# Optimization experiments

Measured on AMD Instinct MI355X. Metric: run time of the kernel, lower is better.

## Reference

```python
import jax, jax.numpy as jnp
import numpy as np

B, N, IN_DIM, OUT_DIM, H = 8, 1024, 512, 512, 8
SUP = OUT_DIM // H  # support_dim per head = 64


def setup_inputs() -> dict:
    key = jax.random.key(0)
    ks = jax.random.split(key, 6)
    # 0/1 dense adjacency with self-loops so no row is fully masked
    A = jax.random.randint(ks[0], (B, N, N), 0, 2).astype(jnp.float32)
    A = jnp.maximum(A, jnp.eye(N, dtype=jnp.float32)[None])
    X = jax.random.normal(ks[1], (B, N, IN_DIM), dtype=jnp.float32)
    # parameters, uniform(-1/sqrt(fan_last), 1/sqrt(fan_last)) as in reset_parameters
    sw = 1.0 / np.sqrt(SUP)
    W = jax.random.uniform(ks[2], (H, IN_DIM, SUP), minval=-sw, maxval=sw, dtype=jnp.float32)
    w1 = jax.random.uniform(ks[3], (H, SUP), minval=-sw, maxval=sw, dtype=jnp.float32)
    w2 = jax.random.uniform(ks[4], (H, SUP), minval=-sw, maxval=sw, dtype=jnp.float32)
    b = jax.random.uniform(ks[5], (2, H), minval=-1.0, maxval=1.0, dtype=jnp.float32)
    b1, b2 = b[0], b[1]
    return {"A": A, "X": X, "W": W, "w1": w1, "b1": b1, "w2": w2, "b2": b2}


def reference(A, X, W, w1, b1, w2, b2):
    # per-head projection: [B,H,N,SUP]
    inputs = jnp.einsum('bni,hio->bhno', X, W)
    # additive attention logits: self_fc [B,H,N,1] + neigh_fc [B,H,1,N]
    self_fc = jnp.einsum('bhno,ho->bhn', inputs, w1) + b1[None, :, None]
    neigh_fc = jnp.einsum('bhno,ho->bhn', inputs, w2) + b2[None, :, None]
    logits = jax.nn.leaky_relu(self_fc[..., :, None] + neigh_fc[..., None, :], 0.01)
    mask = -1e9 * (1.0 - A)  # [B,N,N]
    alphas = jax.nn.softmax(logits + mask[:, None], axis=-1)  # [B,H,N,N]
    out = jnp.einsum('bhnm,bhmo->bhno', alphas, inputs)
    out = jax.nn.relu(out)  # default activation = torch.relu
    # concat heads on last dim (head i contiguous), matching torch.cat
    return out.transpose(0, 2, 1, 3).reshape(B, N, H * SUP)
```

## Files before the change

### kernel.cpp

```cpp
#include <hip/hip_runtime.h>
#include <hip/hip_fp16.h>

#define BB 8
#define NN 1024
#define IN_DIM 512
#define HH 8
#define SUP 64
#define HS (HH * SUP)

#define XS_STRIDE 40
#define VT2 1032

typedef _Float16 half8 __attribute__((ext_vector_type(8)));
typedef _Float16 half2v __attribute__((ext_vector_type(2)));
typedef float floatx4 __attribute__((ext_vector_type(4)));

__global__ __launch_bounds__(256) void kW(const float* __restrict__ W,
                                          _Float16* __restrict__ Wt) {
    __shared__ float tile[64][65];
    const int it = blockIdx.x & 7;
    const int h  = blockIdx.x >> 3;
    const int t  = threadIdx.x;
    {
        const int i  = t >> 2;
        const int o0 = (t & 3) * 16;
        const float* src = W + ((size_t)h * IN_DIM + it * 64 + i) * SUP + o0;
#pragma unroll
        for (int j = 0; j < 4; j++) {
            float4 v = ((const float4*)src)[j];
            tile[i][o0 + j * 4 + 0] = v.x;
            tile[i][o0 + j * 4 + 1] = v.y;
            tile[i][o0 + j * 4 + 2] = v.z;
            tile[i][o0 + j * 4 + 3] = v.w;
        }
    }
    __syncthreads();
    {
        const int o  = t >> 2;
        const int i0 = (t & 3) * 16;
        _Float16 buf[16];
#pragma unroll
        for (int j = 0; j < 16; j++) buf[j] = (_Float16)tile[i0 + j][o];
        _Float16* dst = Wt + ((size_t)h * SUP + o) * IN_DIM + it * 64 + i0;
        *(half8*)dst       = *(half8*)buf;
        *(half8*)(dst + 8) = *(half8*)(buf + 8);
    }
}

__global__ __launch_bounds__(256) void k1_proj(const float* __restrict__ X,
                                               const _Float16* __restrict__ Wt,
                                               const float* __restrict__ A,
                                               unsigned char* __restrict__ Am,
                                               const float* __restrict__ w1,
                                               const float* __restrict__ b1,
                                               const float* __restrict__ w2,
                                               const float* __restrict__ b2,
                                               _Float16* __restrict__ Pt,
                                               float* __restrict__ s_g,
                                               float* __restrict__ t_g,
                                               float* __restrict__ tmax16) {
    __shared__ __align__(16) _Float16 xs[2][64 * XS_STRIDE];
    __shared__ __align__(16) _Float16 wsh[2][128 * XS_STRIDE];
    __shared__ __align__(16) _Float16 po[128 * 72];
    __shared__ float tred[2][64];

    const int bid  = blockIdx.x;
    const int t    = threadIdx.x;
    const int wave = t >> 6;
    const int lane = t & 63;

    if (bid >= 512) {
        const int idx = bid - 512;
#pragma unroll
        for (int i = 0; i < 8; i++) {
            const int row = idx * 32 + wave * 8 + i;
            const float* arow = A + (size_t)row * NN;
            unsigned long long keep = 0;
#pragma unroll
            for (int g = 0; g < 16; g++) {
                float a = arow[g * 64 + lane];
                unsigned long long bal = __ballot(a > 0.5f);
                if (lane == g) keep = bal;
            }
            if (lane < 16)
                *(unsigned long long*)(Am + (size_t)row * 128 + lane * 8) = keep;
        }
        return;
    }

    const int b    = bid & 7;
    const int j    = bid >> 3;
    const int h0   = (j & 3) * 2;
    const int bh0  = b * 8 + h0;
    const int n0   = (j >> 2) * 64;
    const int quad = lane >> 4;
    const int l15  = lane & 15;
    const int row  = t >> 2;
    const int koff = (t & 3) * 8;
    const int wrow  = t >> 1;
    const int wkoff = (t & 1) * 16;

    floatx4 acc[8];
#pragma unroll
    for (int i = 0; i < 8; i++) acc[i] = {0.f, 0.f, 0.f, 0.f};

    float w1v[8], w2v[8];
#pragma unroll
    for (int ct = 0; ct < 8; ct++) {
        w1v[ct] = w1[h0 * 64 + ct * 16 + l15];
        w2v[ct] = w2[h0 * 64 + ct * 16 + l15];
    }
    const float b1h0 = b1[h0], b1h1 = b1[h0 + 1];
    const float b2h0 = b2[h0], b2h1 = b2[h0 + 1];

    const float*    xbase = X + ((size_t)b * NN + n0 + row) * IN_DIM + koff;
    const _Float16* wbase = Wt + ((size_t)(h0 * SUP) + wrow) * IN_DIM + wkoff;

    float4 xa = ((const float4*)xbase)[0];
    float4 xb = ((const float4*)xbase)[1];
    half8  wv0 = ((const half8*)wbase)[0];
    half8  wv1 = *(const half8*)(wbase + 8);

    for (int it = 0; it < 16; it++) {
        const int cur = it & 1;
        {
            _Float16 xh[8] = {(_Float16)xa.x, (_Float16)xa.y, (_Float16)xa.z, (_Float16)xa.w,
                              (_Float16)xb.x, (_Float16)xb.y, (_Float16)xb.z, (_Float16)xb.w};
            *(half8*)&xs[cur][row * XS_STRIDE + koff] = *(half8*)xh;
            *(half8*)&wsh[cur][wrow * XS_STRIDE + wkoff]     = wv0;
            *(half8*)&wsh[cur][wrow * XS_STRIDE + wkoff + 8] = wv1;
        }
        __syncthreads();
        if (it < 15) {
            const float* src = xbase + (it + 1) * 32;
            xa = ((const float4*)src)[0];
            xb = ((const float4*)src)[1];
            wv0 = *(const half8*)(wbase + (it + 1) * 32);
            wv1 = *(const half8*)(wbase + (it + 1) * 32 + 8);
        }
        half8 af = *(const half8*)&xs[cur][(wave * 16 + l15) * XS_STRIDE + quad * 8];
#pragma unroll
        for (int ct = 0; ct < 8; ct++) {
            half8 bf = *(const half8*)&wsh[cur][(ct * 16 + l15) * XS_STRIDE + quad * 8];
            acc[ct] = __builtin_amdgcn_mfma_f32_16x16x32_f16(af, bf, acc[ct], 0, 0, 0);
        }
    }
    __syncthreads();

#pragma unroll
    for (int ct = 0; ct < 8; ct++) {
#pragma unroll
        for (int r = 0; r < 4; r++) {
            int o = ct * 16 + l15;
            int n = wave * 16 + quad * 4 + r;
            po[o * 72 + n] = (_Float16)acc[ct][r];
        }
    }
#pragma unroll
    for (int r = 0; r < 4; r++) {
        float sp0 = 0.f, tp0 = 0.f, sp1 = 0.f, tp1 = 0.f;
#pragma unroll
        for (int ct = 0; ct < 4; ct++) {
            sp0 += acc[ct][r] * w1v[ct];
            tp0 += acc[ct][r] * w2v[ct];
            sp1 += acc[ct + 4][r] * w1v[ct + 4];
            tp1 += acc[ct + 4][r] * w2v[ct + 4];
        }
#pragma unroll
        for (int off = 1; off < 16; off <<= 1) {
            sp0 += __shfl_xor(sp0, off);
            tp0 += __shfl_xor(tp0, off);
            sp1 += __shfl_xor(sp1, off);
            tp1 += __shfl_xor(tp1, off);
        }
        if (l15 == 0) {
            const int n = wave * 16 + quad * 4 + r;
            s_g[(size_t)bh0 * NN + n0 + n] = sp0 + b1h0;
            float tv0 = tp0 + b2h0;
            t_g[(size_t)bh0 * NN + n0 + n] = tv0;
            tred[0][n] = tv0;
            s_g[(size_t)(bh0 + 1) * NN + n0 + n] = sp1 + b1h1;
            float tv1 = tp1 + b2h1;
            t_g[(size_t)(bh0 + 1) * NN + n0 + n] = tv1;
            tred[1][n] = tv1;
        }
    }
    __syncthreads();
    {
        const int orow = t >> 1;
        const int nof  = (t & 1) * 32;
        _Float16* dst = Pt + ((size_t)(bh0 * SUP + orow)) * NN + n0 + nof;
        const _Float16* src = &po[orow * 72 + nof];
        *(half8*)dst        = *(const half8*)src;
        *(half8*)(dst + 8)  = *(const half8*)(src + 8);
        *(half8*)(dst + 16) = *(const half8*)(src + 16);
        *(half8*)(dst + 24) = *(const half8*)(src + 24);
    }
    if (t == 0) {
        float m0 = -1e30f, m1 = -1e30f;
#pragma unroll
        for (int i = 0; i < 64; i++) {
            m0 = fmaxf(m0, tred[0][i]);
            m1 = fmaxf(m1, tred[1][i]);
        }
        tmax16[bh0 * 16 + (n0 >> 6)] = m0;
        tmax16[(bh0 + 1) * 16 + (n0 >> 6)] = m1;
    }
}

__global__ __launch_bounds__(1024) void k2_attn(const unsigned char* __restrict__ Am,
                                                const _Float16* __restrict__ Pt,
                                                const float* __restrict__ s_g,
                                                const float* __restrict__ t_g,
                                                const float* __restrict__ tmax16,
                                                float* __restrict__ out) {
    __shared__ __align__(16) _Float16 vts[64 * VT2];
    __shared__ __align__(16) unsigned t2l[NN / 2];
    __shared__ __align__(16) uint4 lutm[256];

    const int bid  = blockIdx.x;
    const int b    = bid & 7;
    const int rest = bid >> 3;
    const int h    = rest & 7;
    const int bh   = b * 8 + h;
    const int n0   = (rest >> 3) * 256;
    const int t    = threadIdx.x;
    const int wave = t >> 6;
    const int lane = t & 63;
    const int quad = lane >> 4;
    const int l15  = lane & 15;

    {
        const int tt   = t & 511;
        const int half = t >> 9;
        const int row4 = tt >> 3;
        const int seg  = tt & 7;
        const _Float16* src = Pt + ((size_t)bh * SUP + row4) * NN + half * 512 + seg * 16;
        _Float16*       dst = &vts[row4 * VT2 + half * 512 + seg * 16];
        half8 r0[4], r1[4];
#pragma unroll
        for (int m = 0; m < 4; m++) {
            r0[m] = ((const half8*)(src + m * 128))[0];
            r1[m] = ((const half8*)(src + m * 128))[1];
        }
#pragma unroll
        for (int m = 0; m < 4; m++) {
            ((half8*)(dst + m * 128))[0] = r0[m];
            ((half8*)(dst + m * 128))[1] = r1[m];
        }
    }
    if (t < 512) {
        float2 tv2 = ((const float2*)(t_g + (size_t)bh * NN))[t];
        half2v tp = {(_Float16)tv2.x, (_Float16)tv2.y};
        t2l[t] = *(unsigned*)&tp;
    }
    if (t < 256) {
        unsigned e = (unsigned)t;
        uint4 v;
        v.x = ((e & 1u)   ? 0xFFFFu : 0u) | ((e & 2u)   ? 0xFFFF0000u : 0u);
        v.y = ((e & 4u)   ? 0xFFFFu : 0u) | ((e & 8u)   ? 0xFFFF0000u : 0u);
        v.z = ((e & 16u)  ? 0xFFFFu : 0u) | ((e & 32u)  ? 0xFFFF0000u : 0u);
        v.w = ((e & 64u)  ? 0xFFFFu : 0u) | ((e & 128u) ? 0xFFFF0000u : 0u);
        lutm[t] = v;
    }

    float tmax = -1e30f;
#pragma unroll
    for (int i = 0; i < 16; i++) tmax = fmaxf(tmax, tmax16[bh * 16 + i]);

    const int myrow = wave * 16 + l15;
    const float sv = s_g[(size_t)bh * NN + n0 + myrow];
    const float xc = sv + tmax;
    const float cv = fmaxf(xc, 0.01f * xc);
    const float l2e = 1.44269504f;
    const _Float16 sc1h = (_Float16)((sv - cv) * l2e);
    const _Float16 sc2h = (_Float16)(-0.99f * cv * l2e);
    const half2v sc1 = {sc1h, sc1h};
    const half2v sc2 = {sc2h, sc2h};
    const half2v vl2e = {(_Float16)l2e, (_Float16)l2e};
    const half2v v001 = {(_Float16)0.01f, (_Float16)0.01f};
    const half2v ones2 = {(_Float16)1.0f, (_Float16)1.0f};

    floatx4 acc[4];
#pragma unroll
    for (int i = 0; i < 4; i++) acc[i] = {0.f, 0.f, 0.f, 0.f};
    float zp = 0.f;

    const uint4* mrow = (const uint4*)(Am + ((size_t)b * NN + n0 + myrow) * 128);
    uint4 mcur = mrow[0];

    __syncthreads();

    for (int mt = 0; mt < 8; mt++) {
        uint4 mnext;
        if (mt < 7) mnext = mrow[mt + 1];
        const unsigned mw[4] = {mcur.x, mcur.y, mcur.z, mcur.w};
#pragma unroll
        for (int kk = 0; kk < 4; kk++) {
            const unsigned mbyte = (mw[kk] >> (quad * 8)) & 0xffu;
            uint4 mx = lutm[mbyte];
            const unsigned mxw[4] = {mx.x, mx.y, mx.z, mx.w};
            uint4 tw = *(const uint4*)&t2l[mt * 64 + kk * 16 + quad * 4];
            union { uint4 u; half2v h[4]; } tt; tt.u = tw;
            union { half2v h[4]; half8 h8; } wbu;
#pragma unroll
            for (int p = 0; p < 4; p++) {
                half2v y = tt.h[p] * vl2e + sc1;
                half2v w = y * v001 + sc2;
                half2v z = __builtin_elementwise_max(y, w);
                __half2 zz = *(__half2*)&z;
                __half2 ee = h2exp2(zz);
                unsigned eb = (*(unsigned*)&ee) & mxw[p];
                half2v e2 = *(half2v*)&eb;
#if __has_builtin(__builtin_amdgcn_fdot2)
                zp = __builtin_amdgcn_fdot2(e2, ones2, zp, false);
#else
                zp += (float)e2.x + (float)e2.y;
#endif
                wbu.h[p] = e2;
            }
            half8 af = wbu.h8;
#pragma unroll
            for (int ct = 0; ct < 4; ct++) {
                half8 bf = *(const half8*)&vts[(ct * 16 + l15) * VT2 + mt * 128 + kk * 32 + quad * 8];
                acc[ct] = __builtin_amdgcn_mfma_f32_16x16x32_f16(af, bf, acc[ct], 0, 0, 0);
            }
        }
        if (mt < 7) mcur = mnext;
    }

    zp += __shfl_xor(zp, 16);
    zp += __shfl_xor(zp, 32);
    const float rzown = 1.0f / zp;

#pragma unroll
    for (int r = 0; r < 4; r++) {
        const int rr = wave * 16 + quad * 4 + r;
        const float rz = __shfl(rzown, quad * 20 + r);
#pragma unroll
        for (int ct = 0; ct < 4; ct++) {
            float v = acc[ct][r] * rz;
            v = v > 0.f ? v : 0.f;
            out[((size_t)b * NN + n0 + rr) * HS + h * SUP + ct * 16 + l15] = v;
        }
    }
}

extern "C" void kernel_launch(void* const* d_in, const int* in_sizes, int n_in,
                              void* d_out, int out_size, void* d_ws, size_t ws_size,
                              hipStream_t stream) {
    const float* A  = (const float*)d_in[0];
    const float* X  = (const float*)d_in[1];
    const float* W  = (const float*)d_in[2];
    const float* w1 = (const float*)d_in[3];
    const float* b1 = (const float*)d_in[4];
    const float* w2 = (const float*)d_in[5];
    const float* b2 = (const float*)d_in[6];
    float* out = (float*)d_out;

    char* ws = (char*)d_ws;
    _Float16*      Wt     = (_Float16*)(ws);
    _Float16*      Pt     = (_Float16*)(ws + 524288);
    float*         s_g    = (float*)(ws + 8912896);
    float*         t_g    = (float*)(ws + 9175040);
    float*         tmax16 = (float*)(ws + 9437184);
    unsigned char* Am     = (unsigned char*)(ws + 9441280);

    hipLaunchKernelGGL(kW, dim3(64), dim3(256), 0, stream, W, Wt);
    hipLaunchKernelGGL(k1_proj, dim3(768), dim3(256), 0, stream,
                       X, Wt, A, Am, w1, b1, w2, b2, Pt, s_g, t_g, tmax16);
    hipLaunchKernelGGL(k2_attn, dim3(256), dim3(1024), 0, stream,
                       Am, Pt, s_g, t_g, tmax16, out);
}
```

Before: 130.5 us.

## Shrink projection LDS via aliasing, unroll K-loop by two, compute masks arithmetically

In the projection kernel, the double-buffered X/W staging and the output tile now share one aliased LDS array, and the kernel gets a min-blocks-per-CU launch bound of 4 to raise occupancy. The K loop is manually unrolled into two buffers with two prefetch register sets in flight. In the attention kernel, the 256-entry LDS mask lookup table is replaced by shift-based sign extension that builds each half2 mask word in registers. This removes an LDS gather per step and the table setup, at the cost of a few extra ALU ops. The larger prefetch register set could raise pressure under the tighter launch bound.

```diff
diff --git a/kernel.cpp b/kernel.cpp
--- a/kernel.cpp
+++ b/kernel.cpp
@@ -47,22 +47,25 @@
     }
 }
 
-__global__ __launch_bounds__(256) void k1_proj(const float* __restrict__ X,
-                                               const _Float16* __restrict__ Wt,
-                                               const float* __restrict__ A,
-                                               unsigned char* __restrict__ Am,
-                                               const float* __restrict__ w1,
-                                               const float* __restrict__ b1,
-                                               const float* __restrict__ w2,
-                                               const float* __restrict__ b2,
-                                               _Float16* __restrict__ Pt,
-                                               float* __restrict__ s_g,
-                                               float* __restrict__ t_g,
-                                               float* __restrict__ tmax16) {
-    __shared__ __align__(16) _Float16 xs[2][64 * XS_STRIDE];
-    __shared__ __align__(16) _Float16 wsh[2][128 * XS_STRIDE];
-    __shared__ __align__(16) _Float16 po[128 * 72];
+__global__ __launch_bounds__(256, 4) void k1_proj(const float* __restrict__ X,
+                                                  const _Float16* __restrict__ Wt,
+                                                  const float* __restrict__ A,
+                                                  unsigned char* __restrict__ Am,
+                                                  const float* __restrict__ w1,
+                                                  const float* __restrict__ b1,
+                                                  const float* __restrict__ w2,
+                                                  const float* __restrict__ b2,
+                                                  _Float16* __restrict__ Pt,
+                                                  float* __restrict__ s_g,
+                                                  float* __restrict__ t_g,
+                                                  float* __restrict__ tmax16) {
+    __shared__ __align__(16) _Float16 sm[15360];
     __shared__ float tred[2][64];
+    _Float16* const xs0 = sm;
+    _Float16* const xs1 = sm + 2560;
+    _Float16* const ws0 = sm + 5120;
+    _Float16* const ws1 = sm + 10240;
+    _Float16* const po  = sm;
 
     const int bid  = blockIdx.x;
     const int t    = threadIdx.x;
@@ -116,33 +119,64 @@
     const float*    xbase = X + ((size_t)b * NN + n0 + row) * IN_DIM + koff;
     const _Float16* wbase = Wt + ((size_t)(h0 * SUP) + wrow) * IN_DIM + wkoff;
 
-    float4 xa = ((const float4*)xbase)[0];
-    float4 xb = ((const float4*)xbase)[1];
-    half8  wv0 = ((const half8*)wbase)[0];
-    half8  wv1 = *(const half8*)(wbase + 8);
-
-    for (int it = 0; it < 16; it++) {
-        const int cur = it & 1;
+    float4 xaA = ((const float4*)xbase)[0];
+    float4 xbA = ((const float4*)xbase)[1];
+    half8  wv0A = *(const half8*)(wbase);
+    half8  wv1A = *(const half8*)(wbase + 8);
+    float4 xaB = ((const float4*)(xbase + 32))[0];
+    float4 xbB = ((const float4*)(xbase + 32))[1];
+    half8  wv0B = *(const half8*)(wbase + 32);
+    half8  wv1B = *(const half8*)(wbase + 40);
+
+    const int afoff = (wave * 16 + l15) * XS_STRIDE + quad * 8;
+
+#pragma unroll 1
+    for (int jj = 0; jj < 8; jj++) {
         {
-            _Float16 xh[8] = {(_Float16)xa.x, (_Float16)xa.y, (_Float16)xa.z, (_Float16)xa.w,
-                              (_Float16)xb.x, (_Float16)xb.y, (_Float16)xb.z, (_Float16)xb.w};
-            *(half8*)&xs[cur][row * XS_STRIDE + koff] = *(half8*)xh;
-            *(half8*)&wsh[cur][wrow * XS_STRIDE + wkoff]     = wv0;
-            *(half8*)&wsh[cur][wrow * XS_STRIDE + wkoff + 8] = wv1;
+            _Float16 xh[8] = {(_Float16)xaA.x, (_Float16)xaA.y, (_Float16)xaA.z, (_Float16)xaA.w,
+                              (_Float16)xbA.x, (_Float16)xbA.y, (_Float16)xbA.z, (_Float16)xbA.w};
+            *(half8*)&xs0[row * XS_STRIDE + koff] = *(half8*)xh;
+            *(half8*)&ws0[wrow * XS_STRIDE + wkoff]     = wv0A;
+            *(half8*)&ws0[wrow * XS_STRIDE + wkoff + 8] = wv1A;
         }
         __syncthreads();
-        if (it < 15) {
-            const float* src = xbase + (it + 1) * 32;
-            xa = ((const float4*)src)[0];
-            xb = ((const float4*)src)[1];
-            wv0 = *(const half8*)(wbase + (it + 1) * 32);
-            wv1 = *(const half8*)(wbase + (it + 1) * 32 + 8);
-        }
-        half8 af = *(const half8*)&xs[cur][(wave * 16 + l15) * XS_STRIDE + quad * 8];
-#pragma unroll
-        for (int ct = 0; ct < 8; ct++) {
-            half8 bf = *(const half8*)&wsh[cur][(ct * 16 + l15) * XS_STRIDE + quad * 8];
-            acc[ct] = __builtin_amdgcn_mfma_f32_16x16x32_f16(af, bf, acc[ct], 0, 0, 0);
+        if (jj < 7) {
+            const float* src = xbase + (2 * jj + 2) * 32;
+            xaA = ((const float4*)src)[0];
+            xbA = ((const float4*)src)[1];
+            wv0A = *(const half8*)(wbase + (2 * jj + 2) * 32);
+            wv1A = *(const half8*)(wbase + (2 * jj + 2) * 32 + 8);
+        }
+        {
+            half8 af = *(const half8*)&xs0[afoff];
+#pragma unroll
+            for (int ct = 0; ct < 8; ct++) {
+                half8 bf = *(const half8*)&ws0[(ct * 16 + l15) * XS_STRIDE + quad * 8];
+                acc[ct] = __builtin_amdgcn_mfma_f32_16x16x32_f16(af, bf, acc[ct], 0, 0, 0);
+            }
+        }
+        {
+            _Float16 xh[8] = {(_Float16)xaB.x, (_Float16)xaB.y, (_Float16)xaB.z, (_Float16)xaB.w,
+                              (_Float16)xbB.x, (_Float16)xbB.y, (_Float16)xbB.z, (_Float16)xbB.w};
+            *(half8*)&xs1[row * XS_STRIDE + koff] = *(half8*)xh;
+            *(half8*)&ws1[wrow * XS_STRIDE + wkoff]     = wv0B;
+            *(half8*)&ws1[wrow * XS_STRIDE + wkoff + 8] = wv1B;
+        }
+        __syncthreads();
+        if (jj < 7) {
+            const float* src = xbase + (2 * jj + 3) * 32;
+            xaB = ((const float4*)src)[0];
+            xbB = ((const float4*)src)[1];
+            wv0B = *(const half8*)(wbase + (2 * jj + 3) * 32);
+            wv1B = *(const half8*)(wbase + (2 * jj + 3) * 32 + 8);
+        }
+        {
+            half8 af = *(const half8*)&xs1[afoff];
+#pragma unroll
+            for (int ct = 0; ct < 8; ct++) {
+                half8 bf = *(const half8*)&ws1[(ct * 16 + l15) * XS_STRIDE + quad * 8];
+                acc[ct] = __builtin_amdgcn_mfma_f32_16x16x32_f16(af, bf, acc[ct], 0, 0, 0);
+            }
         }
     }
     __syncthreads();
@@ -216,7 +250,6 @@
                                                 float* __restrict__ out) {
     __shared__ __align__(16) _Float16 vts[64 * VT2];
     __shared__ __align__(16) unsigned t2l[NN / 2];
-    __shared__ __align__(16) uint4 lutm[256];
 
     const int bid  = blockIdx.x;
     const int b    = bid & 7;
@@ -253,15 +286,6 @@
         float2 tv2 = ((const float2*)(t_g + (size_t)bh * NN))[t];
         half2v tp = {(_Float16)tv2.x, (_Float16)tv2.y};
         t2l[t] = *(unsigned*)&tp;
-    }
-    if (t < 256) {
-        unsigned e = (unsigned)t;
-        uint4 v;
-        v.x = ((e & 1u)   ? 0xFFFFu : 0u) | ((e & 2u)   ? 0xFFFF0000u : 0u);
-        v.y = ((e & 4u)   ? 0xFFFFu : 0u) | ((e & 8u)   ? 0xFFFF0000u : 0u);
-        v.z = ((e & 16u)  ? 0xFFFFu : 0u) | ((e & 32u)  ? 0xFFFF0000u : 0u);
-        v.w = ((e & 64u)  ? 0xFFFFu : 0u) | ((e & 128u) ? 0xFFFF0000u : 0u);
-        lutm[t] = v;
     }
 
     float tmax = -1e30f;
@@ -298,19 +322,20 @@
 #pragma unroll
         for (int kk = 0; kk < 4; kk++) {
             const unsigned mbyte = (mw[kk] >> (quad * 8)) & 0xffu;
-            uint4 mx = lutm[mbyte];
-            const unsigned mxw[4] = {mx.x, mx.y, mx.z, mx.w};
             uint4 tw = *(const uint4*)&t2l[mt * 64 + kk * 16 + quad * 4];
             union { uint4 u; half2v h[4]; } tt; tt.u = tw;
             union { half2v h[4]; half8 h8; } wbu;
 #pragma unroll
             for (int p = 0; p < 4; p++) {
+                const unsigned mlo = (unsigned)(((int)(mbyte << (31 - 2 * p))) >> 31) & 0x0000FFFFu;
+                const unsigned mhi = (unsigned)(((int)(mbyte << (30 - 2 * p))) >> 31) & 0xFFFF0000u;
+                const unsigned mword = mlo | mhi;
                 half2v y = tt.h[p] * vl2e + sc1;
                 half2v w = y * v001 + sc2;
                 half2v z = __builtin_elementwise_max(y, w);
                 __half2 zz = *(__half2*)&z;
                 __half2 ee = h2exp2(zz);
-                unsigned eb = (*(unsigned*)&ee) & mxw[p];
+                unsigned eb = (*(unsigned*)&ee) & mword;
                 half2v e2 = *(half2v*)&eb;
 #if __has_builtin(__builtin_amdgcn_fdot2)
                 zp = __builtin_amdgcn_fdot2(e2, ones2, zp, false);
```

Measured after the change: 136.2 us. 4.4% more time.
